# Kernel tuning notes

Measured on AMD Instinct MI355X. Metric: run time of the kernel, lower is better.

Reference implementation:

```python
import jax, jax.numpy as jnp
import numpy as np

N, DIM = 100000, 512
HID = DIM // 2


def _mlp(z, W1, b1, W2, b2):
    # shared scorer: [N, dim] -> [N, 1]
    h = jax.nn.relu(z @ W1 + b1)
    return h @ W2 + b2


def setup_inputs() -> dict:
    key = jax.random.key(0)
    k1, k2, k3, k4 = jax.random.split(key, 4)
    s1 = 1.0 / np.sqrt(DIM)
    s2 = 1.0 / np.sqrt(HID)
    return {
        "z1": jax.random.normal(k1, (N, DIM), dtype=jnp.float32),
        "z2": jax.random.normal(k2, (N, DIM), dtype=jnp.float32),
        "W1": jax.random.normal(k3, (DIM, HID), dtype=jnp.float32) * s1,
        "b1": jnp.zeros((HID,), dtype=jnp.float32),
        "W2": jax.random.normal(k4, (HID, 1), dtype=jnp.float32) * s2,
        "b2": jnp.zeros((1,), dtype=jnp.float32),
    }


def reference(z1, z2, W1, b1, W2, b2):
    x = _mlp(z1, W1, b1, W2, b2)  # [N, 1]
    y = _mlp(z2, W1, b1, W2, b2)  # [N, 1]
    # exp-normalize pair: score_x = e^x / (e^x + e^y) == sigmoid(x - y)
    # computed exactly as in the original (plain exp, no max-subtract)
    e_x = jnp.exp(x)
    e_y = jnp.exp(y)
    denom = e_x + e_y
    score_x = e_x / denom  # [N, 1]
    score_y = e_y / denom  # [N, 1]
    # diag(score) @ z  ==  score * z  (row-wise broadcast scale)
    return score_x * z1 + score_y * z2
```

## Files before the change

### kernel.cpp

```cpp
#include <hip/hip_runtime.h>
#include <hip/hip_bf16.h>
#include <cmath>

#define DIM 512
#define HID 256
#define ROWS_PB 16
#define NCHUNK 16
#define CB 16384

typedef __attribute__((ext_vector_type(8))) short short8;
typedef __attribute__((ext_vector_type(4))) float f32x4;

__device__ __forceinline__ unsigned short f2bf(float f) {
  union { float f; unsigned u; } v; v.f = f;
  unsigned u = v.u;
  return (unsigned short)((u + 0x7FFFu + ((u >> 16) & 1u)) >> 16);
}
__device__ __forceinline__ float bf2f(short h) {
  union { unsigned u; float f; } v;
  v.u = ((unsigned)(unsigned short)h) << 16;
  return v.f;
}

__global__ void w1_swz_kernel(const float* __restrict__ W1,
                              unsigned short* __restrict__ w1s) {
  int tid = blockIdx.x * blockDim.x + threadIdx.x;
  if (tid >= DIM * HID) return;
  int k = tid / HID;
  int c = tid - k * HID;
  w1s[(((k >> 3) * HID) + c) * 8 + (k & 7)] = f2bf(W1[tid]);
}

__device__ __forceinline__ short8 cvt8(const f32x4 p0, const f32x4 p1) {
  short8 r;
  r[0] = (short)f2bf(p0[0]); r[1] = (short)f2bf(p0[1]);
  r[2] = (short)f2bf(p0[2]); r[3] = (short)f2bf(p0[3]);
  r[4] = (short)f2bf(p1[0]); r[5] = (short)f2bf(p1[1]);
  r[6] = (short)f2bf(p1[2]); r[7] = (short)f2bf(p1[3]);
  return r;
}

__device__ __forceinline__ void wcombine(float wa, const short8 a, float wb,
                                         const short8 b, f32x4& o0, f32x4& o1) {
#pragma unroll
  for (int i = 0; i < 4; ++i) {
    o0[i] = wa * bf2f(a[i]) + wb * bf2f(b[i]);
    o1[i] = wa * bf2f(a[i + 4]) + wb * bf2f(b[i + 4]);
  }
}

__global__ __launch_bounds__(256, 2) void fa_main_kernel(
    const float* __restrict__ z1, const float* __restrict__ z2,
    const unsigned short* __restrict__ w1s,
    const float* __restrict__ b1, const float* __restrict__ W2,
    const float* __restrict__ b2, float* __restrict__ out, int n) {
  __shared__ short8 Az[2][NCHUNK][64];
  __shared__ unsigned short Bs[2][CB / 2];
  __shared__ float xs2[2][2][ROWS_PB];

  const int t = threadIdx.x;
  const int w = t >> 6;
  const int l = t & 63;
  const int l15 = l & 15, l16 = l >> 4;
  const int s = w & 1;
  const int h = w >> 1;
  const int row0 = blockIdx.x * ROWS_PB;
  const int myrow = row0 + l15;
  const bool rok = myrow < n;
  const float* zz = s ? z2 : z1;
  const float* ap = zz + (size_t)myrow * DIM + (l16 << 3);
  const f32x4 zf4 = (f32x4){0.f, 0.f, 0.f, 0.f};

  auto STAGE = [&](int cc, int buf) {
    const char* gsrc = (const char*)w1s + cc * CB + l * 16;
    char* ldst = (char*)&Bs[buf][0];
#pragma unroll
    for (int r = 0; r < 4; ++r) {
      const int rr = w + r * 4;
      __builtin_amdgcn_global_load_lds(
          (const __attribute__((address_space(1))) void*)(gsrc + rr * 1024),
          (__attribute__((address_space(3))) void*)(ldst + rr * 1024), 16, 0,
          0);
    }
  };

  STAGE(0, 0);
  __builtin_amdgcn_sched_barrier(0);

  {
    f32x4 pp[8][2];
#pragma unroll
    for (int j = 0; j < 8; ++j) {
      const float* p = ap + ((h * 8 + j) << 5);
      pp[j][0] = rok ? *(const f32x4*)(p) : zf4;
      pp[j][1] = rok ? *(const f32x4*)(p + 4) : zf4;
    }
#pragma unroll
    for (int j = 0; j < 8; ++j)
      Az[s][h * 8 + j][l] = cvt8(pp[j][0], pp[j][1]);
  }
  __syncthreads();

  short8 af[NCHUNK];
#pragma unroll
  for (int c = 0; c < NCHUNK; ++c) af[c] = Az[s][c][l];

  f32x4 acc[8];
#pragma unroll
  for (int f = 0; f < 8; ++f) acc[f] = zf4;

#pragma unroll
  for (int c = 0; c < NCHUNK; ++c) {
    if (c + 1 < NCHUNK) STAGE(c + 1, (c + 1) & 1);
    __builtin_amdgcn_sched_barrier(0);
    const short8* bp =
        (const short8*)&Bs[c & 1][0] + (l16 << 8) + (h << 7) + l15;
#pragma unroll
    for (int f = 0; f < 8; ++f) {
      const short8 bf = bp[f << 4];
      acc[f] =
          __builtin_amdgcn_mfma_f32_16x16x32_bf16(af[c], bf, acc[f], 0, 0, 0);
    }
    __syncthreads();
  }

  float part[4] = {0.f, 0.f, 0.f, 0.f};
#pragma unroll
  for (int f = 0; f < 8; ++f) {
    const int cc = (h << 7) + (f << 4) + l15;
    const float w2v = W2[cc];
    const float b1v = b1[cc];
#pragma unroll
    for (int r = 0; r < 4; ++r) {
      const float hh = acc[f][r] + b1v;
      part[r] += (hh > 0.f) ? hh * w2v : 0.f;
    }
  }
#pragma unroll
  for (int r = 0; r < 4; ++r) {
#pragma unroll
    for (int m = 1; m < 16; m <<= 1) part[r] += __shfl_xor(part[r], m, 16);
  }
  if (l15 == 0) {
#pragma unroll
    for (int r = 0; r < 4; ++r) xs2[s][h][(l16 << 2) + r] = part[r];
  }
  __syncthreads();

  const float x = xs2[0][0][l15] + xs2[0][1][l15];
  const float y = xs2[1][0][l15] + xs2[1][1][l15];
  const float d = y - x;
  const float sx = 1.f / (1.f + __expf(d));
  const float sy = 1.f - sx;
  float* orow = out + (size_t)myrow * DIM + (l16 << 3);
  if (rok) {
#pragma unroll
    for (int j = 0; j < 4; ++j) {
      const int c = (w << 2) + j;
      const short8 a0 = Az[0][c][l];
      const short8 a1 = Az[1][c][l];
      f32x4 o0, o1;
      wcombine(sx, a0, sy, a1, o0, o1);
      *(f32x4*)(orow + (c << 5)) = o0;
      *(f32x4*)(orow + (c << 5) + 4) = o1;
    }
  }
}

extern "C" void kernel_launch(void* const* d_in, const int* in_sizes, int n_in,
                              void* d_out, int out_size, void* d_ws,
                              size_t ws_size, hipStream_t stream) {
  const float* z1 = (const float*)d_in[0];
  const float* z2 = (const float*)d_in[1];
  const float* W1 = (const float*)d_in[2];
  const float* b1 = (const float*)d_in[3];
  const float* W2 = (const float*)d_in[4];
  const float* b2 = (const float*)d_in[5];
  float* out = (float*)d_out;
  const int n = in_sizes[0] / DIM;
  unsigned short* w1s = (unsigned short*)d_ws;

  hipLaunchKernelGGL(w1_swz_kernel, dim3((DIM * HID + 255) / 256), dim3(256),
                     0, stream, W1, w1s);
  const int nwg = (n + ROWS_PB - 1) / ROWS_PB;
  hipLaunchKernelGGL(fa_main_kernel, dim3(nwg), dim3(256), 0, stream, z1, z2,
                     w1s, b1, W2, b2, out, n);
}
```

Baseline: 226.0 us.

## Load W1 fragments directly from global into registers instead of LDS staging

Replaces the double-buffered LDS staging of the swizzled bf16 W1 with direct per-lane global loads into a two-deep register buffer interleaved with the MFMAs. This removes per-chunk workgroup barriers and the 32KB LDS weight buffer. In exchange, each wave fetches its weight fragments from cache independently, which increases L2/L1 traffic and register pressure.

```diff
diff --git a/kernel.cpp b/kernel.cpp
--- a/kernel.cpp
+++ b/kernel.cpp
@@ -6,7 +6,6 @@
 #define HID 256
 #define ROWS_PB 16
 #define NCHUNK 16
-#define CB 16384
 
 typedef __attribute__((ext_vector_type(8))) short short8;
 typedef __attribute__((ext_vector_type(4))) float f32x4;
@@ -52,10 +51,9 @@
 __global__ __launch_bounds__(256, 2) void fa_main_kernel(
     const float* __restrict__ z1, const float* __restrict__ z2,
     const unsigned short* __restrict__ w1s,
-    const float* __restrict__ b1, const float* __restrict__ W2,
-    const float* __restrict__ b2, float* __restrict__ out, int n) {
-  __shared__ short8 Az[2][NCHUNK][64];
-  __shared__ unsigned short Bs[2][CB / 2];
+    const float* __restrict__ bias1, const float* __restrict__ W2,
+    const float* __restrict__ bias2, float* __restrict__ out, int n) {
+  __shared__ short8 Az[2 * NCHUNK * 64];
   __shared__ float xs2[2][2][ROWS_PB];
 
   const int t = threadIdx.x;
@@ -71,22 +69,6 @@
   const float* ap = zz + (size_t)myrow * DIM + (l16 << 3);
   const f32x4 zf4 = (f32x4){0.f, 0.f, 0.f, 0.f};
 
-  auto STAGE = [&](int cc, int buf) {
-    const char* gsrc = (const char*)w1s + cc * CB + l * 16;
-    char* ldst = (char*)&Bs[buf][0];
-#pragma unroll
-    for (int r = 0; r < 4; ++r) {
-      const int rr = w + r * 4;
-      __builtin_amdgcn_global_load_lds(
-          (const __attribute__((address_space(1))) void*)(gsrc + rr * 1024),
-          (__attribute__((address_space(3))) void*)(ldst + rr * 1024), 16, 0,
-          0);
-    }
-  };
-
-  STAGE(0, 0);
-  __builtin_amdgcn_sched_barrier(0);
-
   {
     f32x4 pp[8][2];
 #pragma unroll
@@ -97,31 +79,41 @@
     }
 #pragma unroll
     for (int j = 0; j < 8; ++j)
-      Az[s][h * 8 + j][l] = cvt8(pp[j][0], pp[j][1]);
+      Az[(s * NCHUNK + h * 8 + j) * 64 + l] = cvt8(pp[j][0], pp[j][1]);
   }
   __syncthreads();
 
   short8 af[NCHUNK];
 #pragma unroll
-  for (int c = 0; c < NCHUNK; ++c) af[c] = Az[s][c][l];
+  for (int c = 0; c < NCHUNK; ++c) af[c] = Az[(s * NCHUNK + c) * 64 + l];
 
   f32x4 acc[8];
 #pragma unroll
   for (int f = 0; f < 8; ++f) acc[f] = zf4;
 
+  const short8* gB = (const short8*)w1s;
+  const int bbase = (l16 << 8) + (h << 7) + l15;
+  short8 b0[8], b1[8];
 #pragma unroll
-  for (int c = 0; c < NCHUNK; ++c) {
-    if (c + 1 < NCHUNK) STAGE(c + 1, (c + 1) & 1);
-    __builtin_amdgcn_sched_barrier(0);
-    const short8* bp =
-        (const short8*)&Bs[c & 1][0] + (l16 << 8) + (h << 7) + l15;
+  for (int f = 0; f < 8; ++f) b0[f] = gB[bbase + (f << 4)];
 #pragma unroll
-    for (int f = 0; f < 8; ++f) {
-      const short8 bf = bp[f << 4];
-      acc[f] =
-          __builtin_amdgcn_mfma_f32_16x16x32_bf16(af[c], bf, acc[f], 0, 0, 0);
+  for (int cc = 0; cc < NCHUNK / 2; ++cc) {
+    const int c0 = 2 * cc, c1 = 2 * cc + 1;
+#pragma unroll
+    for (int f = 0; f < 8; ++f) b1[f] = gB[(c1 << 10) + bbase + (f << 4)];
+#pragma unroll
+    for (int f = 0; f < 8; ++f)
+      acc[f] = __builtin_amdgcn_mfma_f32_16x16x32_bf16(af[c0], b0[f], acc[f],
+                                                       0, 0, 0);
+    if (c1 + 1 < NCHUNK) {
+#pragma unroll
+      for (int f = 0; f < 8; ++f)
+        b0[f] = gB[((c1 + 1) << 10) + bbase + (f << 4)];
     }
-    __syncthreads();
+#pragma unroll
+    for (int f = 0; f < 8; ++f)
+      acc[f] = __builtin_amdgcn_mfma_f32_16x16x32_bf16(af[c1], b1[f], acc[f],
+                                                       0, 0, 0);
   }
 
   float part[4] = {0.f, 0.f, 0.f, 0.f};
@@ -129,7 +121,7 @@
   for (int f = 0; f < 8; ++f) {
     const int cc = (h << 7) + (f << 4) + l15;
     const float w2v = W2[cc];
-    const float b1v = b1[cc];
+    const float b1v = bias1[cc];
 #pragma unroll
     for (int r = 0; r < 4; ++r) {
       const float hh = acc[f][r] + b1v;
@@ -157,8 +149,8 @@
 #pragma unroll
     for (int j = 0; j < 4; ++j) {
       const int c = (w << 2) + j;
-      const short8 a0 = Az[0][c][l];
-      const short8 a1 = Az[1][c][l];
+      const short8 a0 = Az[(0 * NCHUNK + c) * 64 + l];
+      const short8 a1 = Az[(1 * NCHUNK + c) * 64 + l];
       f32x4 o0, o1;
       wcombine(sx, a0, sy, a1, o0, o1);
       *(f32x4*)(orow + (c << 5)) = o0;
```

Result: faster. 215.6 us (-4.6%).

## Keep A fragments in registers and stage W1 in quarter-column LDS tiles

Applied to the files above, without the earlier changes.

Each block now handles 32 rows, and each wave owns one 16-row tile of z1 or z2 for all 256 hidden columns. A is loaded with software prefetch and converted to bf16 straight into registers instead of going through an LDS round-trip. W1 is staged in four 64-column quarters of 64KB LDS, and the ReLU/W2 reduction runs after each quarter. The final combine swaps bf16 tiles between paired waves through LDS. This doubles per-block row reuse of W1 but makes W1 staging synchronous, with no double buffering, and raises LDS use, which may reduce occupancy.

```diff
diff --git a/kernel.cpp b/kernel.cpp
--- a/kernel.cpp
+++ b/kernel.cpp
@@ -4,9 +4,8 @@
 
 #define DIM 512
 #define HID 256
-#define ROWS_PB 16
+#define ROWS_PB 32
 #define NCHUNK 16
-#define CB 16384
 
 typedef __attribute__((ext_vector_type(8))) short short8;
 typedef __attribute__((ext_vector_type(4))) float f32x4;
@@ -52,115 +51,144 @@
 __global__ __launch_bounds__(256, 2) void fa_main_kernel(
     const float* __restrict__ z1, const float* __restrict__ z2,
     const unsigned short* __restrict__ w1s,
-    const float* __restrict__ b1, const float* __restrict__ W2,
-    const float* __restrict__ b2, float* __restrict__ out, int n) {
-  __shared__ short8 Az[2][NCHUNK][64];
-  __shared__ unsigned short Bs[2][CB / 2];
-  __shared__ float xs2[2][2][ROWS_PB];
+    const float* __restrict__ bias1, const float* __restrict__ W2,
+    const float* __restrict__ bias2, float* __restrict__ out, int n) {
+  __shared__ char smem[65536 + 256];
+  short8* Bq = (short8*)smem;
+  float* xs = (float*)(smem + 65536);
 
   const int t = threadIdx.x;
   const int w = t >> 6;
   const int l = t & 63;
   const int l15 = l & 15, l16 = l >> 4;
   const int s = w & 1;
-  const int h = w >> 1;
+  const int tile = w >> 1;
   const int row0 = blockIdx.x * ROWS_PB;
-  const int myrow = row0 + l15;
-  const bool rok = myrow < n;
+  int myrow = row0 + tile * 16 + l15;
+  const bool rowok = myrow < n;
+  if (!rowok) myrow = n - 1;
   const float* zz = s ? z2 : z1;
   const float* ap = zz + (size_t)myrow * DIM + (l16 << 3);
-  const f32x4 zf4 = (f32x4){0.f, 0.f, 0.f, 0.f};
-
-  auto STAGE = [&](int cc, int buf) {
-    const char* gsrc = (const char*)w1s + cc * CB + l * 16;
-    char* ldst = (char*)&Bs[buf][0];
-#pragma unroll
-    for (int r = 0; r < 4; ++r) {
-      const int rr = w + r * 4;
+
+  auto STAGE = [&](int q) {
+#pragma unroll
+    for (int i = 0; i < 16; ++i) {
+      const int kg = w + (i << 2);
+      const char* gsrc =
+          (const char*)w1s + ((size_t)(kg * 256 + q * 64 + l) << 4);
       __builtin_amdgcn_global_load_lds(
-          (const __attribute__((address_space(1))) void*)(gsrc + rr * 1024),
-          (__attribute__((address_space(3))) void*)(ldst + rr * 1024), 16, 0,
-          0);
+          (const __attribute__((address_space(1))) void*)gsrc,
+          (__attribute__((address_space(3))) void*)(smem +
+                                                    ((kg * 64 + l) << 4)),
+          16, 0, 0);
     }
   };
 
-  STAGE(0, 0);
-  __builtin_amdgcn_sched_barrier(0);
+  STAGE(0);
+  f32x4 paA[2], paB[2];
+  paA[0] = *(const f32x4*)(ap);
+  paA[1] = *(const f32x4*)(ap + 4);
+  paB[0] = *(const f32x4*)(ap + 32);
+  paB[1] = *(const f32x4*)(ap + 36);
+
+  f32x4 acc[4];
+#pragma unroll
+  for (int f = 0; f < 4; ++f) acc[f] = (f32x4){0.f, 0.f, 0.f, 0.f};
+  float part[4] = {0.f, 0.f, 0.f, 0.f};
+  short8 af[NCHUNK];
+
+  __syncthreads();
+
+#define ACCPART(q)                                                        \
+  {                                                                       \
+    _Pragma("unroll") for (int f = 0; f < 4; ++f) {                       \
+      const int cc = ((q) << 6) + (f << 4) + l15;                         \
+      const float w2v = W2[cc];                                           \
+      const float b1v = bias1[cc];                                        \
+      _Pragma("unroll") for (int r = 0; r < 4; ++r) {                     \
+        const float hh = acc[f][r] + b1v;                                 \
+        part[r] += (hh > 0.f) ? hh * w2v : 0.f;                           \
+        acc[f][r] = 0.f;                                                  \
+      }                                                                   \
+    }                                                                     \
+  }
+
+#pragma unroll
+  for (int c = 0; c < NCHUNK; ++c) {
+    if (c & 1)
+      af[c] = cvt8(paB[0], paB[1]);
+    else
+      af[c] = cvt8(paA[0], paA[1]);
+    if (c + 2 < NCHUNK) {
+      const float* apn = ap + ((c + 2) << 5);
+      if (c & 1) {
+        paB[0] = *(const f32x4*)(apn);
+        paB[1] = *(const f32x4*)(apn + 4);
+      } else {
+        paA[0] = *(const f32x4*)(apn);
+        paA[1] = *(const f32x4*)(apn + 4);
+      }
+    }
+    __builtin_amdgcn_sched_barrier(0);
+    const short8* bp = Bq + ((c << 2) + l16) * 64 + l15;
+#pragma unroll
+    for (int f = 0; f < 4; ++f)
+      acc[f] = __builtin_amdgcn_mfma_f32_16x16x32_bf16(af[c], bp[f << 4],
+                                                       acc[f], 0, 0, 0);
+  }
+  ACCPART(0);
+
+#pragma unroll
+  for (int q = 1; q < 4; ++q) {
+    __syncthreads();
+    STAGE(q);
+    __syncthreads();
+#pragma unroll
+    for (int c = 0; c < NCHUNK; ++c) {
+      const short8* bp = Bq + ((c << 2) + l16) * 64 + l15;
+#pragma unroll
+      for (int f = 0; f < 4; ++f)
+        acc[f] = __builtin_amdgcn_mfma_f32_16x16x32_bf16(af[c], bp[f << 4],
+                                                         acc[f], 0, 0, 0);
+    }
+    ACCPART(q);
+  }
+#undef ACCPART
+
+#pragma unroll
+  for (int r = 0; r < 4; ++r) {
+#pragma unroll
+    for (int m = 1; m < 16; m <<= 1) part[r] += __shfl_xor(part[r], m, 16);
+  }
+
+  __syncthreads();
 
   {
-    f32x4 pp[8][2];
-#pragma unroll
-    for (int j = 0; j < 8; ++j) {
-      const float* p = ap + ((h * 8 + j) << 5);
-      pp[j][0] = rok ? *(const f32x4*)(p) : zf4;
-      pp[j][1] = rok ? *(const f32x4*)(p + 4) : zf4;
-    }
-#pragma unroll
-    for (int j = 0; j < 8; ++j)
-      Az[s][h * 8 + j][l] = cvt8(pp[j][0], pp[j][1]);
+    char* eb = smem + (w << 14) + (l << 4);
+#pragma unroll
+    for (int c = 0; c < NCHUNK; ++c) *(short8*)(eb + (c << 10)) = af[c];
+  }
+  if (l15 == 0) {
+#pragma unroll
+    for (int r = 0; r < 4; ++r)
+      xs[(s << 5) + tile * 16 + (l16 << 2) + r] = part[r];
   }
   __syncthreads();
 
-  short8 af[NCHUNK];
-#pragma unroll
-  for (int c = 0; c < NCHUNK; ++c) af[c] = Az[s][c][l];
-
-  f32x4 acc[8];
-#pragma unroll
-  for (int f = 0; f < 8; ++f) acc[f] = zf4;
-
-#pragma unroll
-  for (int c = 0; c < NCHUNK; ++c) {
-    if (c + 1 < NCHUNK) STAGE(c + 1, (c + 1) & 1);
-    __builtin_amdgcn_sched_barrier(0);
-    const short8* bp =
-        (const short8*)&Bs[c & 1][0] + (l16 << 8) + (h << 7) + l15;
-#pragma unroll
-    for (int f = 0; f < 8; ++f) {
-      const short8 bf = bp[f << 4];
-      acc[f] =
-          __builtin_amdgcn_mfma_f32_16x16x32_bf16(af[c], bf, acc[f], 0, 0, 0);
-    }
-    __syncthreads();
-  }
-
-  float part[4] = {0.f, 0.f, 0.f, 0.f};
-#pragma unroll
-  for (int f = 0; f < 8; ++f) {
-    const int cc = (h << 7) + (f << 4) + l15;
-    const float w2v = W2[cc];
-    const float b1v = b1[cc];
-#pragma unroll
-    for (int r = 0; r < 4; ++r) {
-      const float hh = acc[f][r] + b1v;
-      part[r] += (hh > 0.f) ? hh * w2v : 0.f;
-    }
-  }
-#pragma unroll
-  for (int r = 0; r < 4; ++r) {
-#pragma unroll
-    for (int m = 1; m < 16; m <<= 1) part[r] += __shfl_xor(part[r], m, 16);
-  }
-  if (l15 == 0) {
-#pragma unroll
-    for (int r = 0; r < 4; ++r) xs2[s][h][(l16 << 2) + r] = part[r];
-  }
-  __syncthreads();
-
-  const float x = xs2[0][0][l15] + xs2[0][1][l15];
-  const float y = xs2[1][0][l15] + xs2[1][1][l15];
-  const float d = y - x;
-  const float sx = 1.f / (1.f + __expf(d));
+  const float x = xs[tile * 16 + l15];
+  const float y = xs[32 + tile * 16 + l15];
+  const float sx = 1.f / (1.f + __expf(y - x));
   const float sy = 1.f - sx;
+  const float wOwn = s ? sy : sx;
+  const float wOth = s ? sx : sy;
+  const char* pb = smem + ((w ^ 1) << 14) + (l << 4);
   float* orow = out + (size_t)myrow * DIM + (l16 << 3);
-  if (rok) {
-#pragma unroll
-    for (int j = 0; j < 4; ++j) {
-      const int c = (w << 2) + j;
-      const short8 a0 = Az[0][c][l];
-      const short8 a1 = Az[1][c][l];
+  if (rowok) {
+#pragma unroll
+    for (int c = 0; c < NCHUNK; ++c) {
+      const short8 po = *(const short8*)(pb + (c << 10));
       f32x4 o0, o1;
-      wcombine(sx, a0, sy, a1, o0, o1);
+      wcombine(wOwn, af[c], wOth, po, o0, o1);
       *(f32x4*)(orow + (c << 5)) = o0;
       *(f32x4*)(orow + (c << 5) + 4) = o1;
     }
```

After: 318.6 us. +41.0%, slower.

## Drop LDS activation staging, reload fp32 inputs for exact output combine

Applied to the files above, without the earlier changes.

Each wave now loads its row's full activation slice straight into registers as bf16 MFMA fragments, so the LDS copy of converted activations and the sync that went with it are gone. The output combine re-reads z1 and z2 in fp32 with coalesced float4 accesses instead of using the bf16 LDS copies, which makes the output exact but adds a second global read of the inputs (likely L2 hits). LDS usage shrinks, so occupancy is raised to 3 blocks per CU. The price is higher register pressure from keeping 16 fragments in registers, and half the waves now load the same z rows twice.

```diff
diff --git a/kernel.cpp b/kernel.cpp
--- a/kernel.cpp
+++ b/kernel.cpp
@@ -11,15 +11,13 @@
 typedef __attribute__((ext_vector_type(8))) short short8;
 typedef __attribute__((ext_vector_type(4))) float f32x4;
 
+#define AS1 __attribute__((address_space(1)))
+#define AS3 __attribute__((address_space(3)))
+
 __device__ __forceinline__ unsigned short f2bf(float f) {
   union { float f; unsigned u; } v; v.f = f;
   unsigned u = v.u;
   return (unsigned short)((u + 0x7FFFu + ((u >> 16) & 1u)) >> 16);
-}
-__device__ __forceinline__ float bf2f(short h) {
-  union { unsigned u; float f; } v;
-  v.u = ((unsigned)(unsigned short)h) << 16;
-  return v.f;
 }
 
 __global__ void w1_swz_kernel(const float* __restrict__ W1,
@@ -40,23 +38,13 @@
   return r;
 }
 
-__device__ __forceinline__ void wcombine(float wa, const short8 a, float wb,
-                                         const short8 b, f32x4& o0, f32x4& o1) {
-#pragma unroll
-  for (int i = 0; i < 4; ++i) {
-    o0[i] = wa * bf2f(a[i]) + wb * bf2f(b[i]);
-    o1[i] = wa * bf2f(a[i + 4]) + wb * bf2f(b[i + 4]);
-  }
-}
-
-__global__ __launch_bounds__(256, 2) void fa_main_kernel(
+__global__ __launch_bounds__(256, 3) void fa_main_kernel(
     const float* __restrict__ z1, const float* __restrict__ z2,
     const unsigned short* __restrict__ w1s,
-    const float* __restrict__ b1, const float* __restrict__ W2,
-    const float* __restrict__ b2, float* __restrict__ out, int n) {
-  __shared__ short8 Az[2][NCHUNK][64];
-  __shared__ unsigned short Bs[2][CB / 2];
-  __shared__ float xs2[2][2][ROWS_PB];
+    const float* __restrict__ bias1, const float* __restrict__ W2,
+    const float* __restrict__ bias2, float* __restrict__ out, int n) {
+  __shared__ char smem[2 * CB + 256];
+  float* xs2 = (float*)(smem + 2 * CB);
 
   const int t = threadIdx.x;
   const int w = t >> 6;
@@ -65,62 +53,57 @@
   const int s = w & 1;
   const int h = w >> 1;
   const int row0 = blockIdx.x * ROWS_PB;
-  const int myrow = row0 + l15;
+  int myrow = row0 + l15;
   const bool rok = myrow < n;
+  if (!rok) myrow = n - 1;
   const float* zz = s ? z2 : z1;
   const float* ap = zz + (size_t)myrow * DIM + (l16 << 3);
   const f32x4 zf4 = (f32x4){0.f, 0.f, 0.f, 0.f};
 
   auto STAGE = [&](int cc, int buf) {
     const char* gsrc = (const char*)w1s + cc * CB + l * 16;
-    char* ldst = (char*)&Bs[buf][0];
+    char* ldst = smem + buf * CB;
 #pragma unroll
     for (int r = 0; r < 4; ++r) {
       const int rr = w + r * 4;
       __builtin_amdgcn_global_load_lds(
-          (const __attribute__((address_space(1))) void*)(gsrc + rr * 1024),
-          (__attribute__((address_space(3))) void*)(ldst + rr * 1024), 16, 0,
-          0);
+          (const AS1 void*)(gsrc + rr * 1024),
+          (AS3 void*)(ldst + rr * 1024), 16, 0, 0);
     }
   };
 
   STAGE(0, 0);
   __builtin_amdgcn_sched_barrier(0);
-
-  {
-    f32x4 pp[8][2];
+  short8 af[NCHUNK];
 #pragma unroll
-    for (int j = 0; j < 8; ++j) {
-      const float* p = ap + ((h * 8 + j) << 5);
-      pp[j][0] = rok ? *(const f32x4*)(p) : zf4;
-      pp[j][1] = rok ? *(const f32x4*)(p + 4) : zf4;
+  for (int g = 0; g < 4; ++g) {
+    f32x4 p[4][2];
+#pragma unroll
+    for (int j = 0; j < 4; ++j) {
+      const float* pp = ap + (((g << 2) + j) << 5);
+      p[j][0] = rok ? *(const f32x4*)(pp) : zf4;
+      p[j][1] = rok ? *(const f32x4*)(pp + 4) : zf4;
     }
 #pragma unroll
-    for (int j = 0; j < 8; ++j)
-      Az[s][h * 8 + j][l] = cvt8(pp[j][0], pp[j][1]);
+    for (int j = 0; j < 4; ++j) af[(g << 2) + j] = cvt8(p[j][0], p[j][1]);
   }
-  __syncthreads();
-
-  short8 af[NCHUNK];
-#pragma unroll
-  for (int c = 0; c < NCHUNK; ++c) af[c] = Az[s][c][l];
 
   f32x4 acc[8];
 #pragma unroll
   for (int f = 0; f < 8; ++f) acc[f] = zf4;
+
+  __syncthreads();
 
 #pragma unroll
   for (int c = 0; c < NCHUNK; ++c) {
     if (c + 1 < NCHUNK) STAGE(c + 1, (c + 1) & 1);
     __builtin_amdgcn_sched_barrier(0);
     const short8* bp =
-        (const short8*)&Bs[c & 1][0] + (l16 << 8) + (h << 7) + l15;
+        (const short8*)(smem + (c & 1) * CB) + (l16 << 8) + (h << 7) + l15;
 #pragma unroll
-    for (int f = 0; f < 8; ++f) {
-      const short8 bf = bp[f << 4];
-      acc[f] =
-          __builtin_amdgcn_mfma_f32_16x16x32_bf16(af[c], bf, acc[f], 0, 0, 0);
-    }
+    for (int f = 0; f < 8; ++f)
+      acc[f] = __builtin_amdgcn_mfma_f32_16x16x32_bf16(af[c], bp[f << 4],
+                                                       acc[f], 0, 0, 0);
     __syncthreads();
   }
 
@@ -129,7 +112,7 @@
   for (int f = 0; f < 8; ++f) {
     const int cc = (h << 7) + (f << 4) + l15;
     const float w2v = W2[cc];
-    const float b1v = b1[cc];
+    const float b1v = bias1[cc];
 #pragma unroll
     for (int r = 0; r < 4; ++r) {
       const float hh = acc[f][r] + b1v;
@@ -143,26 +126,31 @@
   }
   if (l15 == 0) {
 #pragma unroll
-    for (int r = 0; r < 4; ++r) xs2[s][h][(l16 << 2) + r] = part[r];
+    for (int r = 0; r < 4; ++r)
+      xs2[((s << 1) + h) * ROWS_PB + (l16 << 2) + r] = part[r];
   }
   __syncthreads();
 
-  const float x = xs2[0][0][l15] + xs2[0][1][l15];
-  const float y = xs2[1][0][l15] + xs2[1][1][l15];
-  const float d = y - x;
-  const float sx = 1.f / (1.f + __expf(d));
-  const float sy = 1.f - sx;
-  float* orow = out + (size_t)myrow * DIM + (l16 << 3);
-  if (rok) {
 #pragma unroll
-    for (int j = 0; j < 4; ++j) {
-      const int c = (w << 2) + j;
-      const short8 a0 = Az[0][c][l];
-      const short8 a1 = Az[1][c][l];
-      f32x4 o0, o1;
-      wcombine(sx, a0, sy, a1, o0, o1);
-      *(f32x4*)(orow + (c << 5)) = o0;
-      *(f32x4*)(orow + (c << 5) + 4) = o1;
+  for (int j = 0; j < 8; ++j) {
+    const int idx = j * 256 + t;
+    const int row = idx >> 7;
+    const int c4 = idx & 127;
+    const int grow = row0 + row;
+    if (grow < n) {
+      const float x = xs2[row] + xs2[ROWS_PB + row];
+      const float y = xs2[2 * ROWS_PB + row] + xs2[3 * ROWS_PB + row];
+      const float sx = 1.f / (1.f + __expf(y - x));
+      const float sy = 1.f - sx;
+      const size_t off = (size_t)grow * DIM + ((size_t)c4 << 2);
+      const f32x4 a4 = *(const f32x4*)(z1 + off);
+      const f32x4 b4 = *(const f32x4*)(z2 + off);
+      f32x4 ov;
+      ov[0] = sx * a4[0] + sy * b4[0];
+      ov[1] = sx * a4[1] + sy * b4[1];
+      ov[2] = sx * a4[2] + sy * b4[2];
+      ov[3] = sx * a4[3] + sy * b4[3];
+      *(f32x4*)(out + off) = ov;
     }
   }
 }
```

Measured after the change: 249.5 us. +10.4%, slower.
